# Kernel optimization log

Hardware: AMD Instinct MI355X
Metric: run time of the kernel (lower is better)

The kernel has to match this reference:

```python
import jax, jax.numpy as jnp
import numpy as np

NA, NM = 200000, 100000
DA, DM = 128, 64
H = 128
E = 1000000


def _lin(x, W, b):
    # torch nn.Linear: y = x @ W.T + b, W: [out, in]
    return x @ W.T + b


def setup_inputs() -> dict:
    key = jax.random.key(0)
    ks = jax.random.split(key, 24)
    s = 0.02
    inp = {
        "x_account": jax.random.normal(ks[0], (NA, DA), jnp.float32),
        "x_merchant": jax.random.normal(ks[1], (NM, DM), jnp.float32),
        "e_am_src": jax.random.randint(ks[2], (E,), 0, NA, jnp.int32),
        "e_am_dst": jax.random.randint(ks[3], (E,), 0, NM, jnp.int32),
        "e_am_w": jax.random.uniform(ks[4], (E,), jnp.float32),
        "e_ma_src": jax.random.randint(ks[5], (E,), 0, NM, jnp.int32),
        "e_ma_dst": jax.random.randint(ks[6], (E,), 0, NA, jnp.int32),
        "e_ma_w": jax.random.uniform(ks[7], (E,), jnp.float32),
        # type_proj
        "Wp_a": s * jax.random.normal(ks[8], (H, DA), jnp.float32),
        "bp_a": jnp.zeros((H,), jnp.float32),
        "Wp_m": s * jax.random.normal(ks[9], (H, DM), jnp.float32),
        "bp_m": jnp.zeros((H,), jnp.float32),
        # rel_linears: account->merchant:txn (in=DA), merchant->account:rev (in=DM)
        "Wr_am": s * jax.random.normal(ks[10], (H, DA), jnp.float32),
        "br_am": jnp.zeros((H,), jnp.float32),
        "Wr_ma": s * jax.random.normal(ks[11], (H, DM), jnp.float32),
        "br_ma": jnp.zeros((H,), jnp.float32),
        # combine MLPs (Linear(2H,H) + ReLU)
        "Wc_a": s * jax.random.normal(ks[12], (H, 2 * H), jnp.float32),
        "bc_a": jnp.zeros((H,), jnp.float32),
        "Wc_m": s * jax.random.normal(ks[13], (H, 2 * H), jnp.float32),
        "bc_m": jnp.zeros((H,), jnp.float32),
        # account_out
        "Wo": s * jax.random.normal(ks[14], (1, H), jnp.float32),
        "bo": jnp.zeros((1,), jnp.float32),
    }
    return inp


def reference(x_account, x_merchant, e_am_src, e_am_dst, e_am_w,
              e_ma_src, e_ma_dst, e_ma_w,
              Wp_a, bp_a, Wp_m, bp_m,
              Wr_am, br_am, Wr_ma, br_ma,
              Wc_a, bc_a, Wc_m, bc_m, Wo, bo):
    # self projection per node type
    proj_a = _lin(x_account, Wp_a, bp_a)   # [NA, H]
    proj_m = _lin(x_merchant, Wp_m, bp_m)  # [NM, H]

    # relation account->merchant: lin(src feats) then SpMM (weighted scatter-add to dst)
    lin_am = _lin(x_account, Wr_am, br_am)                    # [NA, H]
    msg_am = e_am_w[:, None] * lin_am[e_am_src]               # [E, H]
    neigh_m = jax.ops.segment_sum(msg_am, e_am_dst, num_segments=proj_m.shape[0])

    # relation merchant->account
    lin_ma = _lin(x_merchant, Wr_ma, br_ma)                   # [NM, H]
    msg_ma = e_ma_w[:, None] * lin_ma[e_ma_src]               # [E, H]
    neigh_a = jax.ops.segment_sum(msg_ma, e_ma_dst, num_segments=proj_a.shape[0])

    # concat + MLP combine per node type
    h_a = jax.nn.relu(_lin(jnp.concatenate([proj_a, neigh_a], axis=1), Wc_a, bc_a))
    h_m = jax.nn.relu(_lin(jnp.concatenate([proj_m, neigh_m], axis=1), Wc_m, bc_m))
    _ = h_m  # computed in original but only account head is returned

    acct_out = jax.nn.sigmoid(_lin(h_a, Wo, bo))[:, 0]        # [NA]
    return acct_out
```

## Files before the change

kernel.cpp:

```cpp
#include <hip/hip_runtime.h>


typedef __attribute__((ext_vector_type(8))) short short8;
typedef __attribute__((ext_vector_type(4))) float f32x4;

#define PSH 12
#define CAP 32

__device__ inline unsigned short f32_bf16(float f) {
  unsigned int u = __float_as_uint(f);
  u += 0x7FFF + ((u >> 16) & 1);
  return (unsigned short)(u >> 16);
}
__device__ inline unsigned int pk_bf16(float a, float b) {
  return (unsigned int)f32_bf16(a) | ((unsigned int)f32_bf16(b) << 16);
}

__global__ __launch_bounds__(256) void setup_kernel(
    const float* __restrict__ xm, unsigned int* __restrict__ xmbf, int nq,
    const int* __restrict__ src, const int* __restrict__ dst,
    const float* __restrict__ w, int* __restrict__ cursor,
    unsigned int* __restrict__ edges, int E,
    const float* __restrict__ Wp_a, const float* __restrict__ bp_a,
    const float* __restrict__ Wr_ma, const float* __restrict__ br_ma,
    const float* __restrict__ Wc_a, const float* __restrict__ bc_a,
    unsigned short* __restrict__ Wcomb, float* __restrict__ beff,
    float* __restrict__ vbr, int nb_cvt) {
  __shared__ float wc_s[256];
  int b = blockIdx.x;
  int t = threadIdx.x;
  if (b < 128) {
    int col = b;
    wc_s[t] = Wc_a[col * 256 + t];
    __syncthreads();
    int wave = t >> 6, lane = t & 63;
    if (wave < 2) {
      int k = t;
      float acc = 0.f;
#pragma unroll
      for (int j = 0; j < 128; j += 4) {
        float a0 = Wp_a[(j + 0) * 128 + k];
        float a1 = Wp_a[(j + 1) * 128 + k];
        float a2 = Wp_a[(j + 2) * 128 + k];
        float a3 = Wp_a[(j + 3) * 128 + k];
        acc += wc_s[j] * a0 + wc_s[j + 1] * a1 + wc_s[j + 2] * a2 + wc_s[j + 3] * a3;
      }
      Wcomb[col * 192 + k] = f32_bf16(acc);
    } else if (wave == 2) {
      int kk = lane;
      float acc = 0.f;
#pragma unroll
      for (int j = 0; j < 128; j += 4) {
        float a0 = Wr_ma[(j + 0) * 64 + kk];
        float a1 = Wr_ma[(j + 1) * 64 + kk];
        float a2 = Wr_ma[(j + 2) * 64 + kk];
        float a3 = Wr_ma[(j + 3) * 64 + kk];
        acc += wc_s[128 + j] * a0 + wc_s[129 + j] * a1 + wc_s[130 + j] * a2 + wc_s[131 + j] * a3;
      }
      Wcomb[col * 192 + 128 + kk] = f32_bf16(acc);
    } else {
      float v1 = wc_s[lane] * bp_a[lane] + wc_s[lane + 64] * bp_a[lane + 64];
      float v2 = wc_s[128 + lane] * br_ma[lane] + wc_s[192 + lane] * br_ma[lane + 64];
#pragma unroll
      for (int m = 1; m <= 32; m <<= 1) {
        v1 += __shfl_xor(v1, m, 64);
        v2 += __shfl_xor(v2, m, 64);
      }
      if (lane == 0) { beff[col] = v1 + bc_a[col]; vbr[col] = v2; }
    }
    return;
  }
  b -= 128;
  if (b < nb_cvt) {
    int i = b * 256 + t;
    if (i < nq) {
      float4 v = ((const float4*)xm)[i];
      ((uint2*)xmbf)[i] = make_uint2(pk_bf16(v.x, v.y), pk_bf16(v.z, v.w));
    }
    return;
  }
  b -= nb_cvt;
  int slice = b >> 3;
  int p = b & 7;
  int e0 = slice * 4096 + t * 16;
  if (e0 >= E) return;
  if (e0 + 16 <= E) {
    int dv[16], sv[16];
    float wv[16];
#pragma unroll
    for (int q = 0; q < 4; ++q) {
      int4 dq = ((const int4*)(dst + e0))[q];
      int4 sq = ((const int4*)(src + e0))[q];
      float4 wq = ((const float4*)(w + e0))[q];
      dv[q * 4 + 0] = dq.x; dv[q * 4 + 1] = dq.y; dv[q * 4 + 2] = dq.z; dv[q * 4 + 3] = dq.w;
      sv[q * 4 + 0] = sq.x; sv[q * 4 + 1] = sq.y; sv[q * 4 + 2] = sq.z; sv[q * 4 + 3] = sq.w;
      wv[q * 4 + 0] = wq.x; wv[q * 4 + 1] = wq.y; wv[q * 4 + 2] = wq.z; wv[q * 4 + 3] = wq.w;
    }
    unsigned int rec[16];
#pragma unroll
    for (int k = 0; k < 16; ++k) {
      unsigned int q = (unsigned int)fminf(wv[k] * 32768.0f, 32767.0f);
      rec[k] = (unsigned int)sv[k] | (q << 17);
    }
#pragma unroll
    for (int k = 0; k < 16; ++k) {
      int d = dv[k];
      if (((d >> PSH) & 7) != p) continue;
      int idx = atomicAdd(&cursor[d], 1);
      if (idx < CAP) edges[((size_t)d << 5) + idx] = rec[k];
    }
  } else {
    for (int k = 0; k < 16 && e0 + k < E; ++k) {
      int e = e0 + k;
      int d = dst[e];
      if (((d >> PSH) & 7) != p) continue;
      int idx = atomicAdd(&cursor[d], 1);
      if (idx < CAP) {
        unsigned int q = (unsigned int)fminf(w[e] * 32768.0f, 32767.0f);
        edges[((size_t)d << 5) + idx] = (unsigned int)src[e] | (q << 17);
      }
    }
  }
}

__global__ __launch_bounds__(256) void gather_kernel(
    const unsigned int* __restrict__ xmbf, const unsigned int* __restrict__ edges,
    const int* __restrict__ cursor, unsigned int* __restrict__ neighbf,
    float* __restrict__ sumw, int NA) {
  int wave = threadIdx.x >> 6, lane = threadIdx.x & 63;
  int a = blockIdx.x * 4 + wave;
  if (a >= NA) return;
  int half = lane >> 5;
  int fp = lane & 31;
  int cnt = cursor[a];
  if (cnt > CAP) cnt = CAP;
  const unsigned int* eb = edges + ((size_t)a << 5);
  float accx = 0.f, accy = 0.f, ws = 0.f;
  const float wscale = 1.0f / 32768.0f;
  for (int e0 = 0; e0 < cnt; e0 += 8) {
#pragma unroll
    for (int k = 0; k < 4; ++k) {
      int e = e0 + k * 2 + half;
      bool valid = e < cnt;
      unsigned int p = eb[valid ? e : 0];
      float w = valid ? (float)(p >> 17) * wscale : 0.f;
      unsigned int s = p & 0x1ffffu;
      unsigned int xp = xmbf[(size_t)s * 32 + fp];
      float x0 = __uint_as_float(xp << 16);
      float x1 = __uint_as_float(xp & 0xffff0000u);
      accx += w * x0;
      accy += w * x1;
      ws += w;
    }
  }
  accx += __shfl_xor(accx, 32, 64);
  accy += __shfl_xor(accy, 32, 64);
  ws   += __shfl_xor(ws, 32, 64);
  if (half == 0) {
    neighbf[(size_t)a * 32 + fp] = pk_bf16(accx, accy);
    if (fp == 0) sumw[a] = ws;
  }
}

__global__ __launch_bounds__(512) void acct_kernel(
    const float* __restrict__ xa, const unsigned int* __restrict__ neighbf,
    const float* __restrict__ sumw, const unsigned int* __restrict__ Wcomb32,
    const float* __restrict__ beff, const float* __restrict__ vbr,
    const float* __restrict__ Wo, const float* __restrict__ bo,
    float* __restrict__ out, int NA) {
  __shared__ unsigned int B_lds[24 * 128 * 4];
  int tid = threadIdx.x;
#pragma unroll
  for (int it = 0; it < 6; ++it) {
    int i = tid + it * 512;
    int c = i >> 7, col = i & 127;
    uint4 v = ((const uint4*)Wcomb32)[col * 24 + c];
    *((uint4*)&B_lds[i * 4]) = v;
  }
  __syncthreads();

  int wave = tid >> 6, lane = tid & 63;
  int n15 = lane & 15, quad = lane >> 4;
  float bo0 = bo[0];

  union U4 { uint4 u; short8 h; };

#pragma unroll
  for (int tile = 0; tile < 2; ++tile) {
    int rowbase = blockIdx.x * 256 + (wave * 2 + tile) * 16;
    int m = rowbase + n15;
    int mc = min(m, NA - 1);

    U4 afr[6];
    const float* xrow = xa + (size_t)mc * 128 + quad * 8;
#pragma unroll
    for (int s = 0; s < 4; ++s) {
      float4 f0 = ((const float4*)(xrow + s * 32))[0];
      float4 f1 = ((const float4*)(xrow + s * 32))[1];
      afr[s].u = make_uint4(pk_bf16(f0.x, f0.y), pk_bf16(f0.z, f0.w),
                            pk_bf16(f1.x, f1.y), pk_bf16(f1.z, f1.w));
    }
#pragma unroll
    for (int s = 0; s < 2; ++s) {
      afr[4 + s].u = ((const uint4*)(neighbf + (size_t)mc * 32))[s * 4 + quad];
    }

    f32x4 acc[8];
#pragma unroll
    for (int t = 0; t < 8; ++t) acc[t] = (f32x4){0.f, 0.f, 0.f, 0.f};

#pragma unroll
    for (int s = 0; s < 6; ++s) {
#pragma unroll
      for (int t = 0; t < 8; ++t) {
        U4 bfr;
        bfr.u = *((const uint4*)&B_lds[((s * 4 + quad) * 128 + t * 16 + n15) * 4]);
        acc[t] = __builtin_amdgcn_mfma_f32_16x16x32_bf16(afr[s].h, bfr.h, acc[t], 0, 0, 0);
      }
    }

    float sw[4];
#pragma unroll
    for (int r = 0; r < 4; ++r) {
      int grow = rowbase + quad * 4 + r;
      sw[r] = (grow < NA) ? sumw[grow] : 0.f;
    }
    float rowsum[4] = {0.f, 0.f, 0.f, 0.f};
#pragma unroll
    for (int t = 0; t < 8; ++t) {
      int col = t * 16 + n15;
      float be = beff[col], vb = vbr[col], wo = Wo[col];
#pragma unroll
      for (int r = 0; r < 4; ++r) {
        float h = acc[t][r] + be + sw[r] * vb;
        h = fmaxf(h, 0.f);
        rowsum[r] += h * wo;
      }
    }
#pragma unroll
    for (int msk = 1; msk <= 8; msk <<= 1) {
#pragma unroll
      for (int r = 0; r < 4; ++r) rowsum[r] += __shfl_xor(rowsum[r], msk, 64);
    }
    if (n15 == 0) {
#pragma unroll
      for (int r = 0; r < 4; ++r) {
        int grow = rowbase + quad * 4 + r;
        if (grow < NA) out[grow] = 1.0f / (1.0f + __expf(-(rowsum[r] + bo0)));
      }
    }
  }
}

extern "C" void kernel_launch(void* const* d_in, const int* in_sizes, int n_in,
                              void* d_out, int out_size, void* d_ws, size_t ws_size,
                              hipStream_t stream) {
  const float* xa      = (const float*)d_in[0];
  const float* xm      = (const float*)d_in[1];
  const int*   ema_src = (const int*)d_in[5];
  const int*   ema_dst = (const int*)d_in[6];
  const float* ema_w   = (const float*)d_in[7];
  const float* Wp_a    = (const float*)d_in[8];
  const float* bp_a    = (const float*)d_in[9];
  const float* Wr_ma   = (const float*)d_in[14];
  const float* br_ma   = (const float*)d_in[15];
  const float* Wc_a    = (const float*)d_in[16];
  const float* bc_a    = (const float*)d_in[17];
  const float* Wo      = (const float*)d_in[20];
  const float* bo      = (const float*)d_in[21];

  int NA = in_sizes[0] / 128;
  int NM = in_sizes[1] / 64;
  int E  = in_sizes[5];

  char* ws = (char*)d_ws;
  size_t off = 0;
  auto take = [&](size_t bytes) { char* p = ws + off; off = (off + bytes + 255) & ~(size_t)255; return p; };
  unsigned int* neighbf = (unsigned int*)take((size_t)NA * 32 * 4);
  unsigned int* xmbf    = (unsigned int*)take((size_t)NM * 32 * 4);
  float* sumw           = (float*)take((size_t)NA * 4);
  int* cursor           = (int*)take((size_t)NA * 4);
  unsigned int* edges   = (unsigned int*)take((size_t)NA * CAP * 4);
  unsigned short* Wcomb = (unsigned short*)take(128 * 192 * 2);
  float* beff           = (float*)take(128 * 4);
  float* vbr            = (float*)take(128 * 4);

  hipMemsetAsync(cursor, 0, (size_t)NA * 4, stream);

  int nq = NM * 16;
  int nb_cvt = (nq + 255) / 256;
  int nb_sc  = ((E + 4095) / 4096) * 8;
  setup_kernel<<<128 + nb_cvt + nb_sc, 256, 0, stream>>>(
      xm, xmbf, nq, ema_src, ema_dst, ema_w, cursor, edges, E,
      Wp_a, bp_a, Wr_ma, br_ma, Wc_a, bc_a, Wcomb, beff, vbr, nb_cvt);

  int gb = (NA + 3) / 4;
  gather_kernel<<<gb, 256, 0, stream>>>(xmbf, edges, cursor, neighbf, sumw, NA);

  int ab = (NA + 255) / 256;
  acct_kernel<<<ab, 512, 0, stream>>>(xa, neighbf, sumw, (const unsigned int*)Wcomb,
                                      beff, vbr, Wo, bo, (float*)d_out, NA);
}
```

Measured before the change: 340.5 us.

## Fuse neighbor gather into account MFMA kernel, removing intermediate buffers

Removes the separate gather kernel and computes each account row's weighted neighbor sum directly inside the account kernel. Each lane gathers bf16 merchant features straight into the MFMA A-fragment layout, and the per-row weight sum is shared by shuffle. This drops the neighbf/sumw round trip through global memory and one kernel launch. In exchange the gather now runs with 16 rows per wave and a per-lane serial edge loop, which may lower memory-level parallelism and raise register pressure.

```diff
diff --git a/kernel.cpp b/kernel.cpp
--- a/kernel.cpp
+++ b/kernel.cpp
@@ -14,6 +14,16 @@
 }
 __device__ inline unsigned int pk_bf16(float a, float b) {
   return (unsigned int)f32_bf16(a) | ((unsigned int)f32_bf16(b) << 16);
+}
+__device__ inline void fma8(float wE, uint4 v, float* a) {
+  a[0] += wE * __uint_as_float(v.x << 16);
+  a[1] += wE * __uint_as_float(v.x & 0xffff0000u);
+  a[2] += wE * __uint_as_float(v.y << 16);
+  a[3] += wE * __uint_as_float(v.y & 0xffff0000u);
+  a[4] += wE * __uint_as_float(v.z << 16);
+  a[5] += wE * __uint_as_float(v.z & 0xffff0000u);
+  a[6] += wE * __uint_as_float(v.w << 16);
+  a[7] += wE * __uint_as_float(v.w & 0xffff0000u);
 }
 
 __global__ __launch_bounds__(256) void setup_kernel(
@@ -123,48 +133,10 @@
   }
 }
 
-__global__ __launch_bounds__(256) void gather_kernel(
-    const unsigned int* __restrict__ xmbf, const unsigned int* __restrict__ edges,
-    const int* __restrict__ cursor, unsigned int* __restrict__ neighbf,
-    float* __restrict__ sumw, int NA) {
-  int wave = threadIdx.x >> 6, lane = threadIdx.x & 63;
-  int a = blockIdx.x * 4 + wave;
-  if (a >= NA) return;
-  int half = lane >> 5;
-  int fp = lane & 31;
-  int cnt = cursor[a];
-  if (cnt > CAP) cnt = CAP;
-  const unsigned int* eb = edges + ((size_t)a << 5);
-  float accx = 0.f, accy = 0.f, ws = 0.f;
-  const float wscale = 1.0f / 32768.0f;
-  for (int e0 = 0; e0 < cnt; e0 += 8) {
-#pragma unroll
-    for (int k = 0; k < 4; ++k) {
-      int e = e0 + k * 2 + half;
-      bool valid = e < cnt;
-      unsigned int p = eb[valid ? e : 0];
-      float w = valid ? (float)(p >> 17) * wscale : 0.f;
-      unsigned int s = p & 0x1ffffu;
-      unsigned int xp = xmbf[(size_t)s * 32 + fp];
-      float x0 = __uint_as_float(xp << 16);
-      float x1 = __uint_as_float(xp & 0xffff0000u);
-      accx += w * x0;
-      accy += w * x1;
-      ws += w;
-    }
-  }
-  accx += __shfl_xor(accx, 32, 64);
-  accy += __shfl_xor(accy, 32, 64);
-  ws   += __shfl_xor(ws, 32, 64);
-  if (half == 0) {
-    neighbf[(size_t)a * 32 + fp] = pk_bf16(accx, accy);
-    if (fp == 0) sumw[a] = ws;
-  }
-}
-
 __global__ __launch_bounds__(512) void acct_kernel(
-    const float* __restrict__ xa, const unsigned int* __restrict__ neighbf,
-    const float* __restrict__ sumw, const unsigned int* __restrict__ Wcomb32,
+    const float* __restrict__ xa, const unsigned int* __restrict__ xmbf,
+    const unsigned int* __restrict__ edges, const int* __restrict__ cursor,
+    const unsigned int* __restrict__ Wcomb32,
     const float* __restrict__ beff, const float* __restrict__ vbr,
     const float* __restrict__ Wo, const float* __restrict__ bo,
     float* __restrict__ out, int NA) {
@@ -182,6 +154,7 @@
   int wave = tid >> 6, lane = tid & 63;
   int n15 = lane & 15, quad = lane >> 4;
   float bo0 = bo[0];
+  const float wscale = 1.0f / 32768.0f;
 
   union U4 { uint4 u; short8 h; };
 
@@ -191,7 +164,44 @@
     int m = rowbase + n15;
     int mc = min(m, NA - 1);
 
+    int cnt = min(cursor[mc], CAP);
+    const unsigned int* eb = edges + ((size_t)mc << 5);
+    uint4 r0 = ((const uint4*)eb)[0];
+    uint4 r1 = ((const uint4*)eb)[1];
+    unsigned int recs[8] = {r0.x, r0.y, r0.z, r0.w, r1.x, r1.y, r1.z, r1.w};
+    float accA[8] = {0.f, 0.f, 0.f, 0.f, 0.f, 0.f, 0.f, 0.f};
+    float accB[8] = {0.f, 0.f, 0.f, 0.f, 0.f, 0.f, 0.f, 0.f};
+    float wsum = 0.f;
+#pragma unroll
+    for (int e = 0; e < 8; ++e) {
+      if (e < cnt) {
+        unsigned int pr = recs[e];
+        float wE = (float)(pr >> 17) * wscale;
+        const uint4* xr = (const uint4*)(xmbf + (size_t)(pr & 0x1ffffu) * 32);
+        uint4 va = xr[quad];
+        uint4 vb = xr[quad + 4];
+        wsum += wE;
+        fma8(wE, va, accA);
+        fma8(wE, vb, accB);
+      }
+    }
+    for (int e = 8; e < cnt; ++e) {
+      unsigned int pr = eb[e];
+      float wE = (float)(pr >> 17) * wscale;
+      const uint4* xr = (const uint4*)(xmbf + (size_t)(pr & 0x1ffffu) * 32);
+      uint4 va = xr[quad];
+      uint4 vb = xr[quad + 4];
+      wsum += wE;
+      fma8(wE, va, accA);
+      fma8(wE, vb, accB);
+    }
+
     U4 afr[6];
+    afr[4].u = make_uint4(pk_bf16(accA[0], accA[1]), pk_bf16(accA[2], accA[3]),
+                          pk_bf16(accA[4], accA[5]), pk_bf16(accA[6], accA[7]));
+    afr[5].u = make_uint4(pk_bf16(accB[0], accB[1]), pk_bf16(accB[2], accB[3]),
+                          pk_bf16(accB[4], accB[5]), pk_bf16(accB[6], accB[7]));
+
     const float* xrow = xa + (size_t)mc * 128 + quad * 8;
 #pragma unroll
     for (int s = 0; s < 4; ++s) {
@@ -200,10 +210,6 @@
       afr[s].u = make_uint4(pk_bf16(f0.x, f0.y), pk_bf16(f0.z, f0.w),
                             pk_bf16(f1.x, f1.y), pk_bf16(f1.z, f1.w));
     }
-#pragma unroll
-    for (int s = 0; s < 2; ++s) {
-      afr[4 + s].u = ((const uint4*)(neighbf + (size_t)mc * 32))[s * 4 + quad];
-    }
 
     f32x4 acc[8];
 #pragma unroll
@@ -221,10 +227,8 @@
 
     float sw[4];
 #pragma unroll
-    for (int r = 0; r < 4; ++r) {
-      int grow = rowbase + quad * 4 + r;
-      sw[r] = (grow < NA) ? sumw[grow] : 0.f;
-    }
+    for (int r = 0; r < 4; ++r) sw[r] = __shfl(wsum, quad * 4 + r, 64);
+
     float rowsum[4] = {0.f, 0.f, 0.f, 0.f};
 #pragma unroll
     for (int t = 0; t < 8; ++t) {
@@ -276,9 +280,7 @@
   char* ws = (char*)d_ws;
   size_t off = 0;
   auto take = [&](size_t bytes) { char* p = ws + off; off = (off + bytes + 255) & ~(size_t)255; return p; };
-  unsigned int* neighbf = (unsigned int*)take((size_t)NA * 32 * 4);
   unsigned int* xmbf    = (unsigned int*)take((size_t)NM * 32 * 4);
-  float* sumw           = (float*)take((size_t)NA * 4);
   int* cursor           = (int*)take((size_t)NA * 4);
   unsigned int* edges   = (unsigned int*)take((size_t)NA * CAP * 4);
   unsigned short* Wcomb = (unsigned short*)take(128 * 192 * 2);
@@ -294,10 +296,8 @@
       xm, xmbf, nq, ema_src, ema_dst, ema_w, cursor, edges, E,
       Wp_a, bp_a, Wr_ma, br_ma, Wc_a, bc_a, Wcomb, beff, vbr, nb_cvt);
 
-  int gb = (NA + 3) / 4;
-  gather_kernel<<<gb, 256, 0, stream>>>(xmbf, edges, cursor, neighbf, sumw, NA);
-
   int ab = (NA + 255) / 256;
-  acct_kernel<<<ab, 512, 0, stream>>>(xa, neighbf, sumw, (const unsigned int*)Wcomb,
+  acct_kernel<<<ab, 512, 0, stream>>>(xa, xmbf, edges, cursor,
+                                      (const unsigned int*)Wcomb,
                                       beff, vbr, Wo, bo, (float*)d_out, NA);
 }
```

Result: faster. 317.4 us (-6.8%).
